# Performance work log

Measured on AMD Instinct MI355X. Metric: run time of the kernel, lower is better.

Reference implementation:

```python
import jax, jax.numpy as jnp
import numpy as np

NUM_TRAITS = 5
NUM_MODALITIES = 3
K = 8
EPS = 1e-08


def setup_inputs() -> dict:
    key = jax.random.key(0)
    k1, k2, k3, k4 = jax.random.split(key, 4)
    labeled_embeddings = jax.random.normal(k1, (20000, NUM_MODALITIES, 256), dtype=jnp.float32)
    labeled_traits = jax.random.uniform(k2, (20000, NUM_TRAITS), dtype=jnp.float32)
    unlabeled_embeddings = jax.random.normal(k3, (2048, NUM_MODALITIES, 256), dtype=jnp.float32)
    trait_modality_logits = jax.random.normal(k4, (NUM_TRAITS, NUM_MODALITIES), dtype=jnp.float32)
    return {
        'labeled_embeddings': labeled_embeddings,
        'labeled_traits': labeled_traits,
        'unlabeled_embeddings': unlabeled_embeddings,
        'trait_modality_logits': trait_modality_logits,
    }


def reference(labeled_embeddings, labeled_traits, unlabeled_embeddings, trait_modality_logits):
    # L2-normalize along feature dim (eps added to norm, matching torch code)
    lab_norm = labeled_embeddings / (jnp.linalg.norm(labeled_embeddings, axis=-1, keepdims=True) + EPS)
    unl_norm = unlabeled_embeddings / (jnp.linalg.norm(unlabeled_embeddings, axis=-1, keepdims=True) + EPS)

    # per-modality cosine similarity: [U, M, L]
    modality_sim = jnp.einsum('umd,lmd->uml', unl_norm, lab_norm)

    # per-trait modality weights and weighted similarity: [U, T, L]
    modality_weights = jax.nn.softmax(trait_modality_logits, axis=-1)  # [T, M]
    combined_sim = jnp.einsum('tm,uml->utl', modality_weights, modality_sim)

    # top-k neighbors per (query, trait)
    _, neighbor_indices = jax.lax.top_k(combined_sim, K)  # [U, T, K]

    # gather modality embeddings for neighbors: [U, T, K, M, D]
    neighbor_embeddings = labeled_embeddings[neighbor_indices]

    # gather the trait value corresponding to each trait head: [U, T, K]
    trait_ids = jnp.arange(NUM_TRAITS)[None, :, None]  # [1, T, 1]
    neighbor_traits = labeled_traits[neighbor_indices, trait_ids]

    return neighbor_embeddings, neighbor_traits, neighbor_indices.astype(jnp.int64)
```

## Files before the change

kernel.cpp:

```cpp
#include <hip/hip_runtime.h>
#include <hip/hip_bf16.h>
#include <math.h>

#define L_CNT 20000
#define U_CNT 2048
#define M_CNT 3
#define D_CNT 256
#define KTOT  768
#define T_CNT 5
#define K_OUT 8
#define KC    16
#define LP    20096
#define LROWS (L_CNT*M_CNT)
#define UROWS (U_CNT*M_CNT)
#define CHUNKS 313
#define CPAD   320

typedef unsigned short ushort_t;
typedef unsigned int uint_t;
typedef __attribute__((ext_vector_type(8))) short bf16x8;
typedef __attribute__((ext_vector_type(4))) float f32x4;

__device__ inline double dshfl_xor(double v, int m){
    long long x = __double_as_longlong(v);
    int lo = (int)(x & 0xffffffffLL);
    int hi = (int)(((unsigned long long)x) >> 32);
    lo = __shfl_xor(lo, m, 64);
    hi = __shfl_xor(hi, m, 64);
    return __longlong_as_double(((long long)hi << 32) | (long long)(unsigned int)lo);
}
__device__ inline unsigned short f2bf(float f){
    unsigned int u = __float_as_uint(f);
    u = (u + 0x7fffu + ((u >> 16) & 1u)) >> 16;
    return (unsigned short)u;
}
__device__ __forceinline__ void gload16(const void* g, void* l){
    __builtin_amdgcn_global_load_lds(
        (const __attribute__((address_space(1))) unsigned int*)g,
        (__attribute__((address_space(3))) unsigned int*)l, 16, 0, 0);
}
__device__ __forceinline__ float h2f(ushort_t h){
    _Float16 x; __builtin_memcpy(&x, &h, 2); return (float)x;
}
__device__ __forceinline__ ushort_t f2h(float f){
    _Float16 hv = (_Float16)f;
    ushort_t b; __builtin_memcpy(&b, &hv, 2);
    return b;
}
__device__ __forceinline__ ushort_t f2key(float f){
    ushort_t b = f2h(f);
    ushort_t mask = (ushort_t)(0x8000u | (((short)b >> 15) & 0x7FFF));
    return (ushort_t)(b ^ mask);
}
__device__ __forceinline__ ushort_t get16(const uint4& v, int e){
    uint_t w = (e < 2) ? v.x : (e < 4) ? v.y : (e < 6) ? v.z : v.w;
    return (ushort_t)((e & 1) ? (w >> 16) : (w & 0xFFFFu));
}
__device__ __forceinline__ float comb3(float w0, float w1, float w2, float a, float b, float c){
    return fmaf(w2, c, fmaf(w1, b, w0*a));
}
__device__ __forceinline__ void radix_find(uint_t hist[4][256], uint_t* h1, uint_t* h2,
    int tid, uint_t addBase, uint_t kc, uint_t* shB, uint_t* shAbove)
{
    h1[tid] = hist[0][tid]+hist[1][tid]+hist[2][tid]+hist[3][tid];
    uint_t* src = h1; uint_t* dst = h2;
    for (int st=1; st<256; st<<=1){
        __syncthreads();
        dst[tid] = src[tid] + ((tid+st < 256) ? src[tid+st] : 0u);
        uint_t* tt = src; src = dst; dst = tt;
    }
    __syncthreads();
    uint_t ge = src[tid] + addBase;
    uint_t gt = ((tid < 255) ? src[tid+1] : 0u) + addBase;
    if (ge >= kc && gt < kc){ *shB = (uint_t)tid; *shAbove = gt; }
    __syncthreads();
}

__global__ __launch_bounds__(256) void prep_kernel(const float* __restrict__ lab,
    const float* __restrict__ unl, const float* __restrict__ logits,
    double* __restrict__ invL64, double* __restrict__ invU64,
    ushort_t* __restrict__ labN, ushort_t* __restrict__ unlN,
    float* __restrict__ w32, double* __restrict__ w64){
    if (blockIdx.x == 0 && threadIdx.x < T_CNT){
        int t = threadIdx.x;
        float a = logits[t*M_CNT+0], b = logits[t*M_CNT+1], c = logits[t*M_CNT+2];
        float mx = fmaxf(a, fmaxf(b, c));
        float e0 = expf(a-mx), e1 = expf(b-mx), e2 = expf(c-mx);
        float s = e0+e1+e2;
        w32[t*M_CNT+0] = e0/s; w32[t*M_CNT+1] = e1/s; w32[t*M_CNT+2] = e2/s;
        double da=(double)a, db=(double)b, dc=(double)c;
        double dmx = fmax(da, fmax(db, dc));
        double f0 = exp(da-dmx), f1 = exp(db-dmx), f2 = exp(dc-dmx);
        double ds = f0+f1+f2;
        w64[t*M_CNT+0] = f0/ds; w64[t*M_CNT+1] = f1/ds; w64[t*M_CNT+2] = f2/ds;
    }
    const int NROW = LROWS + UROWS;
    int row = blockIdx.x*4 + (threadIdx.x >> 6);
    int lane = threadIdx.x & 63;
    if (row >= NROW) return;
    bool isLab = row < LROWS;
    const float* p = isLab ? (lab + (size_t)row*D_CNT) : (unl + (size_t)(row-LROWS)*D_CNT);
    float4 a = ((const float4*)p)[lane];
    double sS = (double)a.x*a.x + (double)a.y*a.y + (double)a.z*a.z + (double)a.w*a.w;
#pragma unroll
    for (int m=1;m<64;m<<=1) sS += dshfl_xor(sS, m);
    double inv = 1.0/(sqrt(sS) + 1e-8);
    if (lane == 0){
        if (isLab) invL64[row] = inv;
        else invU64[row-LROWS] = inv;
    }
    float sc = (float)inv;
    ushort4 o;
    o.x = f2bf(a.x*sc); o.y = f2bf(a.y*sc); o.z = f2bf(a.z*sc); o.w = f2bf(a.w*sc);
    ushort_t* dst = isLab ? (labN + (size_t)row*D_CNT) : (unlN + (size_t)(row-LROWS)*D_CNT);
    *(ushort4*)&dst[lane*4] = o;
}

__global__ __launch_bounds__(256, 2) void sim_kernel(
    const ushort_t* __restrict__ labN, const ushort_t* __restrict__ unlN,
    const float* __restrict__ w32, ushort_t* __restrict__ slabp,
    ushort_t* __restrict__ chunkMax)
{
    __shared__ ushort_t sA[128][64];
    __shared__ ushort_t sB[128][64];
    __shared__ float    sT[64][132];

    const int tid  = threadIdx.x;
    const int lane = tid & 63;
    const int w    = tid >> 6;
    const int wu = w >> 1, wl = w & 1;
    const int fr = lane & 15, fg = lane >> 4;

    const int uB = blockIdx.x * 128;
    const int l0 = blockIdx.y * 128;

    const int sr   = lane >> 3;
    const int scol = ((lane & 7) ^ sr) * 8;
    const ushort_t* pA[4]; const ushort_t* pB[4];
    ushort_t* dA[4]; ushort_t* dB[4];
#pragma unroll
    for (int g=0; g<4; g++){
        int ar = uB + g*32 + w*8 + sr;
        pA[g] = unlN + (size_t)ar*KTOT + scol;
        dA[g] = &sA[g*32 + w*8][0];
        int br = l0 + g*32 + w*8 + sr; if (br > L_CNT-1) br = L_CNT-1;
        pB[g] = labN + (size_t)br*KTOT + scol;
        dB[g] = &sB[g*32 + w*8][0];
    }

    int aoff[4][2], boff[4][2];
#pragma unroll
    for (int i=0;i<4;i++)
#pragma unroll
        for (int ks=0;ks<2;ks++){
            int sw = ((ks*4 + fg) ^ (fr & 7)) * 16;
            aoff[i][ks] = (wu*64 + i*16 + fr)*128 + sw;
            boff[i][ks] = (wl*64 + i*16 + fr)*128 + sw;
        }

    uint4 hA[2][4], hB[2][4];

#pragma unroll
    for (int m=0; m<M_CNT; m++){
        f32x4 acc[4][4];
#pragma unroll
        for (int i=0;i<4;i++)
#pragma unroll
            for (int j=0;j<4;j++) acc[i][j] = (f32x4){0.f,0.f,0.f,0.f};

#pragma unroll
        for (int kb=0; kb<4; kb++){
            const int koff = (m*4 + kb) * 64;
            __syncthreads();
#pragma unroll
            for (int g=0; g<4; g++){
                gload16(pA[g] + koff, dA[g]);
                gload16(pB[g] + koff, dB[g]);
            }
            __syncthreads();
#pragma unroll
            for (int ks=0; ks<2; ks++){
                bf16x8 af[4], bf[4];
#pragma unroll
                for (int i=0;i<4;i++) af[i] = *(const bf16x8*)((const char*)sA + aoff[i][ks]);
#pragma unroll
                for (int j=0;j<4;j++) bf[j] = *(const bf16x8*)((const char*)sB + boff[j][ks]);
#pragma unroll
                for (int i=0;i<4;i++)
#pragma unroll
                    for (int j=0;j<4;j++)
                        acc[i][j] = __builtin_amdgcn_mfma_f32_16x16x32_bf16(af[i], bf[j], acc[i][j], 0, 0, 0);
            }
        }

        float wl5[T_CNT][3];
        if (m == 2){
#pragma unroll
            for (int t=0;t<T_CNT;t++)
#pragma unroll
                for (int j=0;j<3;j++) wl5[t][j] = w32[t*3+j];
        }

#pragma unroll
        for (int half=0; half<2; half++){
            __syncthreads();
            if (wu == half){
#pragma unroll
                for (int i=0;i<4;i++)
#pragma unroll
                    for (int j=0;j<4;j++)
#pragma unroll
                        for (int r=0;r<4;r++)
                            sT[i*16 + fg*4 + r][wl*64 + j*16 + fr] = acc[i][j][r];
            }
            __syncthreads();
            const int c0 = (tid & 15) * 8;
#pragma unroll
            for (int it=0; it<4; it++){
                int row = it*16 + (tid >> 4);
                ushort_t h[8];
#pragma unroll
                for (int e=0;e<8;e++) h[e] = f2h(sT[row][c0 + e]);
                uint4 hv = *(const uint4*)h;
                size_t base = ((size_t)(uB + half*64 + row)*M_CNT + m)*LP + l0 + c0;
                *(uint4*)&slabp[base] = hv;

                if (m == 0) hA[half][it] = hv;
                else if (m == 1) hB[half][it] = hv;
                else {
                    uint_t rm[T_CNT] = {0,0,0,0,0};
#pragma unroll
                    for (int e=0;e<8;e++){
                        int l = l0 + c0 + e;
                        float a = h2f(get16(hA[half][it], e));
                        float b = h2f(get16(hB[half][it], e));
                        float c = h2f(get16(hv, e));
                        if (l < L_CNT){
#pragma unroll
                            for (int t=0;t<T_CNT;t++){
                                uint_t k = f2key(comb3(wl5[t][0],wl5[t][1],wl5[t][2], a,b,c));
                                rm[t] = (k > rm[t]) ? k : rm[t];
                            }
                        }
                    }
#pragma unroll
                    for (int t=0;t<T_CNT;t++){
                        uint_t k = rm[t], o;
                        o = (uint_t)__shfl_xor((int)k, 1, 64); k = (o > k) ? o : k;
                        o = (uint_t)__shfl_xor((int)k, 2, 64); k = (o > k) ? o : k;
                        o = (uint_t)__shfl_xor((int)k, 4, 64); k = (o > k) ? o : k;
                        rm[t] = k;
                    }
                    if ((tid & 7) == 0){
                        int chunkc = (l0 >> 6) + ((tid >> 3) & 1);
                        if (chunkc < CHUNKS){
                            int ug = uB + half*64 + row;
#pragma unroll
                            for (int t=0;t<T_CNT;t++)
                                chunkMax[((size_t)ug*T_CNT + t)*CPAD + chunkc] = (ushort_t)rm[t];
                        }
                    }
                }
            }
        }
        __syncthreads();
    }
}

__global__ __launch_bounds__(256) void select2_kernel(
    const ushort_t* __restrict__ slabp, const ushort_t* __restrict__ chunkMax,
    const float* __restrict__ w32, int* __restrict__ candIdx)
{
    __shared__ ushort_t mxs[CPAD];
    __shared__ ushort_t cand[CPAD];
    __shared__ uint_t hist[4][256];
    __shared__ uint_t h1[256], h2[256];
    __shared__ uint_t shB, shAbove, shNc, shCtr0, shCtr1;
    __shared__ int bufc[KC];

    const int tid = threadIdx.x, wid = tid >> 6;
    const int u = blockIdx.x, t = blockIdx.y;
    const float w0 = w32[t*3+0], w1 = w32[t*3+1], w2 = w32[t*3+2];
    const ushort_t* s0 = slabp + ((size_t)u*M_CNT + 0)*LP;
    const ushort_t* s1 = slabp + ((size_t)u*M_CNT + 1)*LP;
    const ushort_t* s2 = slabp + ((size_t)u*M_CNT + 2)*LP;
    const ushort_t* cm = chunkMax + ((size_t)u*T_CNT + t)*CPAD;

    for (int i=tid; i<CPAD; i+=256) mxs[i] = (i < CHUNKS) ? cm[i] : (ushort_t)0;
    hist[0][tid]=0; hist[1][tid]=0; hist[2][tid]=0; hist[3][tid]=0;
    if (tid == 0){ shNc = 0; shCtr0 = 0; shCtr1 = 0; }
    __syncthreads();

    for (int i=tid; i<CHUNKS; i+=256) atomicAdd(&hist[wid][mxs[i] >> 8], 1u);
    __syncthreads();
    radix_find(hist, h1, h2, tid, 0u, KC, &shB, &shAbove);
    const uint_t MB = shB, mAb = shAbove;
    hist[0][tid]=0; hist[1][tid]=0; hist[2][tid]=0; hist[3][tid]=0;
    __syncthreads();
    for (int i=tid; i<CHUNKS; i+=256){
        uint_t k = mxs[i];
        if ((k >> 8) == MB) atomicAdd(&hist[wid][k & 0xFFu], 1u);
    }
    __syncthreads();
    radix_find(hist, h1, h2, tid, mAb, KC, &shB, &shAbove);
    const uint_t tau = (MB << 8) | shB;
    hist[0][tid]=0; hist[1][tid]=0; hist[2][tid]=0; hist[3][tid]=0;
    __syncthreads();

    for (int i=tid; i<CHUNKS; i+=256)
        if ((uint_t)mxs[i] >= tau) cand[atomicAdd(&shNc, 1u)] = (ushort_t)i;
    __syncthreads();
    const int NE = (int)shNc * 64;

    for (int j=tid; j<NE; j+=256){
        int l = (int)cand[j>>6]*64 + (j & 63);
        if (l < L_CNT){
            uint_t k = f2key(comb3(w0,w1,w2, h2f(s0[l]), h2f(s1[l]), h2f(s2[l])));
            atomicAdd(&hist[wid][k >> 8], 1u);
        }
    }
    __syncthreads();
    radix_find(hist, h1, h2, tid, 0u, KC, &shB, &shAbove);
    const uint_t EB = shB, eAb = shAbove;
    hist[0][tid]=0; hist[1][tid]=0; hist[2][tid]=0; hist[3][tid]=0;
    __syncthreads();

    for (int j=tid; j<NE; j+=256){
        int l = (int)cand[j>>6]*64 + (j & 63);
        if (l < L_CNT){
            uint_t k = f2key(comb3(w0,w1,w2, h2f(s0[l]), h2f(s1[l]), h2f(s2[l])));
            if ((k >> 8) == EB) atomicAdd(&hist[wid][k & 0xFFu], 1u);
        }
    }
    __syncthreads();
    radix_find(hist, h1, h2, tid, eAb, KC, &shB, &shAbove);
    const uint_t K16 = (EB << 8) | shB;
    const uint_t tot = shAbove;

    for (int j=tid; j<NE; j+=256){
        int l = (int)cand[j>>6]*64 + (j & 63);
        if (l < L_CNT){
            uint_t k = f2key(comb3(w0,w1,w2, h2f(s0[l]), h2f(s1[l]), h2f(s2[l])));
            if (k > K16){
                bufc[atomicAdd(&shCtr0, 1u)] = l;
            } else if (k == K16){
                uint_t s = atomicAdd(&shCtr1, 1u) + tot;
                if (s < (uint_t)KC) bufc[s] = l;
            }
        }
    }
    __syncthreads();
    if (tid < KC) candIdx[((size_t)u*T_CNT + t)*KC + tid] = bufc[tid];
}

__global__ __launch_bounds__(256) void rescore_kernel(
    const float* __restrict__ lab, const float* __restrict__ unl,
    const double* __restrict__ w64, const double* __restrict__ invL64,
    const double* __restrict__ invU64, const int* __restrict__ candIdx,
    double* __restrict__ candSim)
{
    int q = blockIdx.x*4 + (threadIdx.x >> 6);
    int lane = threadIdx.x & 63;
    int ut = q >> 4;
    int t = ut % T_CNT;
    int u = ut / T_CNT;
    int idx = candIdx[q];
    double p = 0.0;
#pragma unroll
    for (int m=0;m<M_CNT;m++){
        double s = w64[t*M_CNT+m] * invU64[u*M_CNT+m] * invL64[idx*M_CNT+m];
        float4 a = *(const float4*)&unl[(((size_t)u*M_CNT)+m)*D_CNT + lane*4];
        float4 b = *(const float4*)&lab[(((size_t)idx*M_CNT)+m)*D_CNT + lane*4];
        double d = (double)a.x*b.x + (double)a.y*b.y + (double)a.z*b.z + (double)a.w*b.w;
        p += s * d;
    }
#pragma unroll
    for (int mm=1;mm<64;mm<<=1) p += dshfl_xor(p, mm);
    if (lane == 0) candSim[q] = p;
}

__global__ __launch_bounds__(256) void finalize_kernel(
    const double* __restrict__ candSim, const int* __restrict__ candIdx,
    const float* __restrict__ traits,
    float* __restrict__ outTraits, float* __restrict__ outIdx, int* __restrict__ finalIdx)
{
    int id = blockIdx.x*256 + threadIdx.x;
    if (id >= U_CNT*T_CNT) return;
    int t = id % T_CNT;
    double cv[KC]; int ci[KC];
#pragma unroll
    for (int c=0;c<KC;c++){ cv[c] = candSim[(size_t)id*KC + c]; ci[c] = candIdx[(size_t)id*KC + c]; }
#pragma unroll
    for (int i=0;i<KC;i++)
#pragma unroll
        for (int j=0;j<KC-1;j++){
            bool sw = (cv[j] < cv[j+1]) || (cv[j] == cv[j+1] && ci[j] > ci[j+1]);
            if (sw){ double tv=cv[j]; cv[j]=cv[j+1]; cv[j+1]=tv; int ti=ci[j]; ci[j]=ci[j+1]; ci[j+1]=ti; }
        }
#pragma unroll
    for (int k=0;k<K_OUT;k++){
        size_t ob = (size_t)id*K_OUT + k;
        int fi = ci[k];
        outTraits[ob] = traits[(size_t)fi*T_CNT + t];
        outIdx[ob] = (float)fi;
        finalIdx[ob] = fi;
    }
}

__global__ __launch_bounds__(192) void gather_kernel(const float* __restrict__ lab,
    const int* __restrict__ finalIdx, float* __restrict__ outEmb)
{
    int b = blockIdx.x;
    int idx = finalIdx[b];
    const float4* src = (const float4*)(lab + (size_t)idx * (M_CNT*D_CNT));
    float4* dst = (float4*)(outEmb + (size_t)b * (M_CNT*D_CNT));
    dst[threadIdx.x] = src[threadIdx.x];
}

extern "C" void kernel_launch(void* const* d_in, const int* in_sizes, int n_in,
                              void* d_out, int out_size, void* d_ws, size_t ws_size,
                              hipStream_t stream) {
    const float* lab    = (const float*)d_in[0];
    const float* traits = (const float*)d_in[1];
    const float* unl    = (const float*)d_in[2];
    const float* logits = (const float*)d_in[3];

    float* out = (float*)d_out;
    float* outEmb = out;
    float* outTr  = out + (size_t)U_CNT*T_CNT*K_OUT*M_CNT*D_CNT;
    float* outIx  = outTr + (size_t)U_CNT*T_CNT*K_OUT;

    char* wsb = (char*)d_ws;
    size_t off = 0;
    auto take = [&](size_t bytes)->void*{
        void* p = wsb + off;
        off = (off + bytes + 255) & ~(size_t)255;
        return p;
    };
    double* invL64 = (double*)take((size_t)LROWS*sizeof(double));
    double* invU64 = (double*)take((size_t)UROWS*sizeof(double));
    float*  w32    = (float*) take(T_CNT*M_CNT*sizeof(float));
    double* w64    = (double*)take(T_CNT*M_CNT*sizeof(double));
    int*    candIdx= (int*)   take((size_t)U_CNT*T_CNT*KC*sizeof(int));
    double* candSim= (double*)take((size_t)U_CNT*T_CNT*KC*sizeof(double));
    int*    finalIdx=(int*)   take((size_t)U_CNT*T_CNT*K_OUT*sizeof(int));
    ushort_t* labN = (ushort_t*)take((size_t)LROWS*D_CNT*sizeof(ushort_t));
    ushort_t* unlN = (ushort_t*)take((size_t)UROWS*D_CNT*sizeof(ushort_t));
    ushort_t* chunkMax = (ushort_t*)take((size_t)U_CNT*T_CNT*CPAD*sizeof(ushort_t));

    ushort_t* slabV = (ushort_t*)outEmb;

    {
        int nrow = LROWS + UROWS;
        prep_kernel<<<(nrow+3)/4, 256, 0, stream>>>(lab, unl, logits, invL64, invU64, labN, unlN, w32, w64);
    }
    sim_kernel<<<dim3(U_CNT/128, (L_CNT + 127)/128), 256, 0, stream>>>(labN, unlN, w32, slabV, chunkMax);
    select2_kernel<<<dim3(U_CNT, T_CNT), 256, 0, stream>>>(slabV, chunkMax, w32, candIdx);
    rescore_kernel<<<(U_CNT*T_CNT*KC)/4, 256, 0, stream>>>(lab, unl, w64, invL64, invU64, candIdx, candSim);
    finalize_kernel<<<(U_CNT*T_CNT + 255)/256, 256, 0, stream>>>(candSim, candIdx, traits, outTr, outIx, finalIdx);
    gather_kernel<<<U_CNT*T_CNT*K_OUT, 192, 0, stream>>>(lab, finalIdx, outEmb);
}
```

Measured before the change: 408.5 us.

## Fuse rescore, finalize and gather into one per-query kernel; float chunk max

Replaces the separate rescore, finalize (sort) and gather kernels with a single kernel per (query, trait). Each block rescores its 16 candidates in FP64, sorts them in shared memory, writes traits and indices, then copies the 8 neighbor embedding rows. This removes the candSim/finalIdx round trips through global memory and two kernel launches. The sim kernel also now takes its per-chunk max in float and converts to a key once at the end, instead of converting every element to a key before the max. The cost is a serial single-thread sort inside each block, which leaves the other threads idle until it finishes.

```diff
diff --git a/kernel.cpp b/kernel.cpp
--- a/kernel.cpp
+++ b/kernel.cpp
@@ -228,7 +228,9 @@
                 if (m == 0) hA[half][it] = hv;
                 else if (m == 1) hB[half][it] = hv;
                 else {
-                    uint_t rm[T_CNT] = {0,0,0,0,0};
+                    float rmf[T_CNT];
+#pragma unroll
+                    for (int t=0;t<T_CNT;t++) rmf[t] = -INFINITY;
 #pragma unroll
                     for (int e=0;e<8;e++){
                         int l = l0 + c0 + e;
@@ -237,19 +239,17 @@
                         float c = h2f(get16(hv, e));
                         if (l < L_CNT){
 #pragma unroll
-                            for (int t=0;t<T_CNT;t++){
-                                uint_t k = f2key(comb3(wl5[t][0],wl5[t][1],wl5[t][2], a,b,c));
-                                rm[t] = (k > rm[t]) ? k : rm[t];
-                            }
+                            for (int t=0;t<T_CNT;t++)
+                                rmf[t] = fmaxf(rmf[t], comb3(wl5[t][0],wl5[t][1],wl5[t][2], a,b,c));
                         }
                     }
 #pragma unroll
                     for (int t=0;t<T_CNT;t++){
-                        uint_t k = rm[t], o;
-                        o = (uint_t)__shfl_xor((int)k, 1, 64); k = (o > k) ? o : k;
-                        o = (uint_t)__shfl_xor((int)k, 2, 64); k = (o > k) ? o : k;
-                        o = (uint_t)__shfl_xor((int)k, 4, 64); k = (o > k) ? o : k;
-                        rm[t] = k;
+                        float k = rmf[t];
+                        k = fmaxf(k, __shfl_xor(k, 1, 64));
+                        k = fmaxf(k, __shfl_xor(k, 2, 64));
+                        k = fmaxf(k, __shfl_xor(k, 4, 64));
+                        rmf[t] = k;
                     }
                     if ((tid & 7) == 0){
                         int chunkc = (l0 >> 6) + ((tid >> 3) & 1);
@@ -257,7 +257,7 @@
                             int ug = uB + half*64 + row;
 #pragma unroll
                             for (int t=0;t<T_CNT;t++)
-                                chunkMax[((size_t)ug*T_CNT + t)*CPAD + chunkc] = (ushort_t)rm[t];
+                                chunkMax[((size_t)ug*T_CNT + t)*CPAD + chunkc] = f2key(rmf[t]);
                         }
                     }
                 }
@@ -353,68 +353,75 @@
     if (tid < KC) candIdx[((size_t)u*T_CNT + t)*KC + tid] = bufc[tid];
 }
 
-__global__ __launch_bounds__(256) void rescore_kernel(
+__global__ __launch_bounds__(256) void rfg_kernel(
     const float* __restrict__ lab, const float* __restrict__ unl,
     const double* __restrict__ w64, const double* __restrict__ invL64,
     const double* __restrict__ invU64, const int* __restrict__ candIdx,
-    double* __restrict__ candSim)
+    const float* __restrict__ traits,
+    float* __restrict__ outEmb, float* __restrict__ outTraits, float* __restrict__ outIdx)
 {
-    int q = blockIdx.x*4 + (threadIdx.x >> 6);
-    int lane = threadIdx.x & 63;
-    int ut = q >> 4;
-    int t = ut % T_CNT;
-    int u = ut / T_CNT;
-    int idx = candIdx[q];
-    double p = 0.0;
-#pragma unroll
-    for (int m=0;m<M_CNT;m++){
-        double s = w64[t*M_CNT+m] * invU64[u*M_CNT+m] * invL64[idx*M_CNT+m];
-        float4 a = *(const float4*)&unl[(((size_t)u*M_CNT)+m)*D_CNT + lane*4];
-        float4 b = *(const float4*)&lab[(((size_t)idx*M_CNT)+m)*D_CNT + lane*4];
-        double d = (double)a.x*b.x + (double)a.y*b.y + (double)a.z*b.z + (double)a.w*b.w;
-        p += s * d;
-    }
-#pragma unroll
-    for (int mm=1;mm<64;mm<<=1) p += dshfl_xor(p, mm);
-    if (lane == 0) candSim[q] = p;
-}
-
-__global__ __launch_bounds__(256) void finalize_kernel(
-    const double* __restrict__ candSim, const int* __restrict__ candIdx,
-    const float* __restrict__ traits,
-    float* __restrict__ outTraits, float* __restrict__ outIdx, int* __restrict__ finalIdx)
-{
-    int id = blockIdx.x*256 + threadIdx.x;
-    if (id >= U_CNT*T_CNT) return;
-    int t = id % T_CNT;
-    double cv[KC]; int ci[KC];
-#pragma unroll
-    for (int c=0;c<KC;c++){ cv[c] = candSim[(size_t)id*KC + c]; ci[c] = candIdx[(size_t)id*KC + c]; }
-#pragma unroll
-    for (int i=0;i<KC;i++)
-#pragma unroll
-        for (int j=0;j<KC-1;j++){
-            bool sw = (cv[j] < cv[j+1]) || (cv[j] == cv[j+1] && ci[j] > ci[j+1]);
-            if (sw){ double tv=cv[j]; cv[j]=cv[j+1]; cv[j+1]=tv; int ti=ci[j]; ci[j]=ci[j+1]; ci[j+1]=ti; }
-        }
-#pragma unroll
-    for (int k=0;k<K_OUT;k++){
-        size_t ob = (size_t)id*K_OUT + k;
-        int fi = ci[k];
-        outTraits[ob] = traits[(size_t)fi*T_CNT + t];
-        outIdx[ob] = (float)fi;
-        finalIdx[ob] = fi;
-    }
-}
-
-__global__ __launch_bounds__(192) void gather_kernel(const float* __restrict__ lab,
-    const int* __restrict__ finalIdx, float* __restrict__ outEmb)
-{
-    int b = blockIdx.x;
-    int idx = finalIdx[b];
-    const float4* src = (const float4*)(lab + (size_t)idx * (M_CNT*D_CNT));
-    float4* dst = (float4*)(outEmb + (size_t)b * (M_CNT*D_CNT));
-    dst[threadIdx.x] = src[threadIdx.x];
+    __shared__ double sval[KC];
+    __shared__ int sidx[KC];
+    __shared__ int finals[K_OUT];
+
+    const int ut = blockIdx.x;
+    const int t = ut % T_CNT, u = ut / T_CNT;
+    const int tid = threadIdx.x;
+    const int wv = tid >> 6, lane = tid & 63;
+
+    float4 av[3];
+    double su[3];
+#pragma unroll
+    for (int m=0;m<3;m++){
+        av[m] = *(const float4*)&unl[(((size_t)u*M_CNT)+m)*D_CNT + lane*4];
+        su[m] = w64[t*M_CNT+m] * invU64[u*M_CNT+m];
+    }
+
+#pragma unroll
+    for (int c=0;c<4;c++){
+        int q = wv*4 + c;
+        int idx = candIdx[(size_t)ut*KC + q];
+        double p = 0.0;
+#pragma unroll
+        for (int m=0;m<3;m++){
+            float4 b = *(const float4*)&lab[(((size_t)idx*M_CNT)+m)*D_CNT + lane*4];
+            double d = (double)av[m].x*b.x + (double)av[m].y*b.y + (double)av[m].z*b.z + (double)av[m].w*b.w;
+            p += (su[m] * invL64[idx*M_CNT+m]) * d;
+        }
+#pragma unroll
+        for (int mm=1;mm<64;mm<<=1) p += dshfl_xor(p, mm);
+        if (lane == 0){ sval[q] = p; sidx[q] = idx; }
+    }
+    __syncthreads();
+
+    if (tid == 0){
+        double cv[KC]; int ci[KC];
+#pragma unroll
+        for (int c=0;c<KC;c++){ cv[c] = sval[c]; ci[c] = sidx[c]; }
+#pragma unroll
+        for (int i=0;i<KC;i++)
+#pragma unroll
+            for (int j=0;j<KC-1;j++){
+                bool sw = (cv[j] < cv[j+1]) || (cv[j] == cv[j+1] && ci[j] > ci[j+1]);
+                if (sw){ double tv=cv[j]; cv[j]=cv[j+1]; cv[j+1]=tv; int ti=ci[j]; ci[j]=ci[j+1]; ci[j+1]=ti; }
+            }
+#pragma unroll
+        for (int k=0;k<K_OUT;k++){
+            int fi = ci[k];
+            finals[k] = fi;
+            size_t ob = (size_t)ut*K_OUT + k;
+            outTraits[ob] = traits[(size_t)fi*T_CNT + t];
+            outIdx[ob] = (float)fi;
+        }
+    }
+    __syncthreads();
+
+    for (int it = tid; it < K_OUT*192; it += 256){
+        int k = it / 192, o = it % 192;
+        int fi = finals[k];
+        float4 v = ((const float4*)(lab + (size_t)fi*(M_CNT*D_CNT)))[o];
+        ((float4*)(outEmb + ((size_t)ut*K_OUT + k)*(M_CNT*D_CNT)))[o] = v;
+    }
 }
 
 extern "C" void kernel_launch(void* const* d_in, const int* in_sizes, int n_in,
@@ -442,8 +449,6 @@
     float*  w32    = (float*) take(T_CNT*M_CNT*sizeof(float));
     double* w64    = (double*)take(T_CNT*M_CNT*sizeof(double));
     int*    candIdx= (int*)   take((size_t)U_CNT*T_CNT*KC*sizeof(int));
-    double* candSim= (double*)take((size_t)U_CNT*T_CNT*KC*sizeof(double));
-    int*    finalIdx=(int*)   take((size_t)U_CNT*T_CNT*K_OUT*sizeof(int));
     ushort_t* labN = (ushort_t*)take((size_t)LROWS*D_CNT*sizeof(ushort_t));
     ushort_t* unlN = (ushort_t*)take((size_t)UROWS*D_CNT*sizeof(ushort_t));
     ushort_t* chunkMax = (ushort_t*)take((size_t)U_CNT*T_CNT*CPAD*sizeof(ushort_t));
@@ -456,7 +461,5 @@
     }
     sim_kernel<<<dim3(U_CNT/128, (L_CNT + 127)/128), 256, 0, stream>>>(labN, unlN, w32, slabV, chunkMax);
     select2_kernel<<<dim3(U_CNT, T_CNT), 256, 0, stream>>>(slabV, chunkMax, w32, candIdx);
-    rescore_kernel<<<(U_CNT*T_CNT*KC)/4, 256, 0, stream>>>(lab, unl, w64, invL64, invU64, candIdx, candSim);
-    finalize_kernel<<<(U_CNT*T_CNT + 255)/256, 256, 0, stream>>>(candSim, candIdx, traits, outTr, outIx, finalIdx);
-    gather_kernel<<<U_CNT*T_CNT*K_OUT, 192, 0, stream>>>(lab, finalIdx, outEmb);
-}
+    rfg_kernel<<<U_CNT*T_CNT, 256, 0, stream>>>(lab, unl, w64, invL64, invU64, candIdx, traits, outEmb, outTr, outIx);
+}
```

Result: slower. 430.7 us (+5.4%).
